# Kernel tuning notes

Hardware: AMD Instinct MI355X
Metric: run time of the kernel (lower is better)

The kernel has to match this reference:

```python
import jax, jax.numpy as jnp
import numpy as np
import math

N = 65536
C_IN = 64
C_OUT = 64
NS = 16
BN_EPS = 1e-5


def _knn_idx(p_np, k):
    # exact kNN (including self), chunked to bound memory
    p_np = np.asarray(p_np, np.float32)
    n = p_np.shape[0]
    sq = (p_np * p_np).sum(1)
    idx = np.empty((n, k), np.int32)
    cs = 1024
    for s in range(0, n, cs):
        q = p_np[s:s + cs]
        d = sq[None, :] - 2.0 * (q @ p_np.T) + (q * q).sum(1)[:, None]
        part = np.argpartition(d, k, axis=1)[:, :k]
        dd = np.take_along_axis(d, part, 1)
        order = np.argsort(dd, axis=1)
        idx[s:s + cs] = np.take_along_axis(part, order, 1).astype(np.int32)
    return idx


def setup_inputs() -> dict:
    key = jax.random.key(0)
    ks = jax.random.split(key, 12)
    p = jax.random.uniform(ks[0], (N, 3), dtype=jnp.float32) * 10.0
    x = jax.random.normal(ks[1], (N, C_IN), dtype=jnp.float32)
    idx = jnp.asarray(_knn_idx(np.asarray(p), NS))  # (N, NS) int32
    s_in = 1.0 / math.sqrt(C_IN)
    Wq = jax.random.normal(ks[2], (C_IN, C_OUT), dtype=jnp.float32) * s_in
    bq = jnp.zeros((C_OUT,), jnp.float32)
    Wk = jax.random.normal(ks[3], (C_IN, C_OUT), dtype=jnp.float32) * s_in
    bk = jnp.zeros((C_OUT,), jnp.float32)
    Wv = jax.random.normal(ks[4], (C_IN, C_OUT), dtype=jnp.float32) * s_in
    bv = jnp.zeros((C_OUT,), jnp.float32)
    Wp1 = jax.random.normal(ks[5], (3, 3), dtype=jnp.float32) * (1.0 / math.sqrt(3))
    bp1 = jnp.zeros((3,), jnp.float32)
    gamma = jnp.ones((3,), jnp.float32)
    beta = jnp.zeros((3,), jnp.float32)
    Wp2 = jax.random.normal(ks[6], (3, C_OUT), dtype=jnp.float32) * (1.0 / math.sqrt(3))
    bp2 = jnp.zeros((C_OUT,), jnp.float32)
    return {"p": p, "x": x, "idx": idx, "Wq": Wq, "bq": bq, "Wk": Wk, "bk": bk,
            "Wv": Wv, "bv": bv, "Wp1": Wp1, "bp1": bp1, "gamma": gamma,
            "beta": beta, "Wp2": Wp2, "bp2": bp2}


def reference(p, x, idx, Wq, bq, Wk, bk, Wv, bv, Wp1, bp1, gamma, beta, Wp2, bp2):
    x_q = x @ Wq + bq                       # (N, Co)
    x_k = (x @ Wk + bk)[idx]                # gather: (N, NS, Co)
    x_v = (x @ Wv + bv)[idx]                # gather: (N, NS, Co)
    p_r = p[idx] - p[:, None, :]            # relative coords (N, NS, 3)
    # linear_p: Linear(3,3) -> BatchNorm1d(3) (training stats) -> ReLU -> Linear(3,Co)
    h = p_r @ Wp1 + bp1                     # (N, NS, 3)
    mean = h.mean(axis=(0, 1))
    var = ((h - mean) ** 2).mean(axis=(0, 1))
    h = (h - mean) * jax.lax.rsqrt(var + BN_EPS) * gamma + beta
    h = jax.nn.relu(h)
    p_emb = h @ Wp2 + bp2                   # (N, NS, Co)
    x_k = x_k + p_emb
    x_v = x_v + p_emb
    attn = (x_q[:, None, :] * x_k).sum(-1) / math.sqrt(C_OUT)  # (N, NS)
    w = jax.nn.softmax(attn, axis=1)
    return (x_v * w[:, :, None]).sum(axis=1)  # (N, Co)
```

## Files before the change

kernel.cpp:

```cpp
#include <hip/hip_runtime.h>

#define N_PTS 65536
#define NSS 16

typedef __attribute__((ext_vector_type(8))) short short8;
typedef __attribute__((ext_vector_type(4))) float f32x4;

__device__ __forceinline__ unsigned short f2bf(float v) {
  unsigned int u = __float_as_uint(v);
  u += 0x7fffu + ((u >> 16) & 1u);
  return (unsigned short)(u >> 16);
}
__device__ __forceinline__ unsigned int pk2(float lo, float hi) {
  return (unsigned int)f2bf(lo) | ((unsigned int)f2bf(hi) << 16);
}
__device__ __forceinline__ float bflo(unsigned int u) { return __uint_as_float(u << 16); }
__device__ __forceinline__ float bfhi(unsigned int u) { return __uint_as_float(u & 0xffff0000u); }

union BF8 { int4 i; short8 s; };
union BU  { ushort4 u[2]; short8 s; };

__global__ __launch_bounds__(256, 3) void qkv_kernel(
    const float* __restrict__ x,
    const float* __restrict__ Wq, const float* __restrict__ Wk, const float* __restrict__ Wv,
    const float* __restrict__ bq, const float* __restrict__ bk, const float* __restrict__ bv,
    const float* __restrict__ Wp2, const float* __restrict__ bp2,
    const float* __restrict__ p, const int* __restrict__ idx,
    unsigned short* __restrict__ kvq, float* __restrict__ tq, float* __restrict__ statsP) {
  __shared__ __align__(16) unsigned short wtl[192 * 68];
  __shared__ __align__(16) unsigned short kvs[64 * 192];
  __shared__ __align__(16) unsigned short b2s[5 * 64];
  const int t = threadIdx.x, blk = blockIdx.x;
  const int p0 = blk * 64;
  const int lane = t & 63, wave = t >> 6;
  const int quad = lane >> 4, lr = lane & 15;

  const int pn = p0 + (t >> 2);
  const int4 j4 = ((const int4*)idx)[pn * 4 + (t & 3)];
  const float pnx = p[pn * 3 + 0], pny = p[pn * 3 + 1], pnz = p[pn * 3 + 2];
  const int js[4] = {j4.x, j4.y, j4.z, j4.w};
  float jx[4], jy[4], jz[4];
#pragma unroll
  for (int i = 0; i < 4; ++i) {
    jx[i] = p[js[i] * 3 + 0]; jy[i] = p[js[i] * 3 + 1]; jz[i] = p[js[i] * 3 + 2];
  }

#pragma unroll 8
  for (int i = 0; i < 48; ++i) {
    const int id = i * 256 + t;
    const int mat = id >> 12, rem = id & 4095;
    const int k = rem >> 6, n = rem & 63;
    const float* W = mat == 0 ? Wq : (mat == 1 ? Wk : Wv);
    wtl[(mat * 64 + n) * 68 + k] = f2bf(W[k * 64 + n]);
  }
  {
    const int row = t >> 6, c = t & 63;
    b2s[t] = f2bf(row < 3 ? Wp2[row * 64 + c] : bp2[c]);
    if (t < 64) b2s[256 + t] = 0;
  }
  __syncthreads();

  const int mrow = p0 + wave * 16 + lr;
  const float* xrow = x + (size_t)mrow * 64;
  const float4 fa = *(const float4*)(xrow + quad * 8);
  const float4 fb = *(const float4*)(xrow + quad * 8 + 4);
  const float4 fc = *(const float4*)(xrow + 32 + quad * 8);
  const float4 fd = *(const float4*)(xrow + 32 + quad * 8 + 4);
  BF8 ua, ub;
  ua.i = make_int4(pk2(fa.x, fa.y), pk2(fa.z, fa.w), pk2(fb.x, fb.y), pk2(fb.z, fb.w));
  ub.i = make_int4(pk2(fc.x, fc.y), pk2(fc.z, fc.w), pk2(fd.x, fd.y), pk2(fd.z, fd.w));
  const short8 a0 = ua.s;
  const short8 a1 = ub.s;

#pragma unroll
  for (int nt = 0; nt < 12; ++nt) {
    const unsigned short* bpr = wtl + (nt * 16 + lr) * 68 + quad * 8;
    BU B0, B1;
    B0.u[0] = *(const ushort4*)bpr;        B0.u[1] = *(const ushort4*)(bpr + 4);
    B1.u[0] = *(const ushort4*)(bpr + 32); B1.u[1] = *(const ushort4*)(bpr + 36);
    f32x4 acc = {0.f, 0.f, 0.f, 0.f};
    acc = __builtin_amdgcn_mfma_f32_16x16x32_bf16(a0, B0.s, acc, 0, 0, 0);
    acc = __builtin_amdgcn_mfma_f32_16x16x32_bf16(a1, B1.s, acc, 0, 0, 0);
    const int mat = nt >> 2;
    const int c = (nt & 3) * 16 + lr;
    const float bias = (mat == 0 ? bq : (mat == 1 ? bk : bv))[c];
#pragma unroll
    for (int r = 0; r < 4; ++r) {
      const int row = wave * 16 + quad * 4 + r;
      kvs[row * 192 + mat * 64 + c] = f2bf(acc[r] + bias);
    }
  }
  {
    const unsigned short* qp = kvs + (wave * 16 + lr) * 192;
    const short8 a0q = *(const short8*)(qp + quad * 8);
    const short8 a1q = *(const short8*)(qp + quad * 8 + 32);
    const unsigned short* b2p = b2s + (lr < 4 ? lr : 4) * 64 + quad * 8;
    const short8 b0q = *(const short8*)b2p;
    const short8 b1q = *(const short8*)(b2p + 32);
    f32x4 acc = {0.f, 0.f, 0.f, 0.f};
    acc = __builtin_amdgcn_mfma_f32_16x16x32_bf16(a0q, b0q, acc, 0, 0, 0);
    acc = __builtin_amdgcn_mfma_f32_16x16x32_bf16(a1q, b1q, acc, 0, 0, 0);
    if (lr < 4) {
#pragma unroll
      for (int r = 0; r < 4; ++r) {
        const int pt = p0 + wave * 16 + quad * 4 + r;
        tq[pt * 4 + lr] = acc[r];
      }
    }
  }

  float s0 = 0, s1 = 0, s2 = 0, s00 = 0, s01 = 0, s02 = 0, s11 = 0, s12 = 0, s22 = 0;
#pragma unroll
  for (int i = 0; i < 4; ++i) {
    const float dx = jx[i] - pnx, dy = jy[i] - pny, dz = jz[i] - pnz;
    s0 += dx; s1 += dy; s2 += dz;
    s00 += dx * dx; s01 += dx * dy; s02 += dx * dz;
    s11 += dy * dy; s12 += dy * dz; s22 += dz * dz;
  }
#pragma unroll
  for (int m = 1; m < 64; m <<= 1) {
    s0 += __shfl_xor(s0, m, 64);  s1 += __shfl_xor(s1, m, 64);  s2 += __shfl_xor(s2, m, 64);
    s00 += __shfl_xor(s00, m, 64); s01 += __shfl_xor(s01, m, 64); s02 += __shfl_xor(s02, m, 64);
    s11 += __shfl_xor(s11, m, 64); s12 += __shfl_xor(s12, m, 64); s22 += __shfl_xor(s22, m, 64);
  }

  __syncthreads();

  const uint4* kvs4 = (const uint4*)kvs;
  uint4* dst = (uint4*)(kvq + (size_t)p0 * 192);
#pragma unroll
  for (int j = 0; j < 6; ++j) dst[j * 256 + t] = kvs4[j * 256 + t];

  float* part = (float*)b2s;
  if (lane == 0) {
    part[wave * 9 + 0] = s0;  part[wave * 9 + 1] = s1;  part[wave * 9 + 2] = s2;
    part[wave * 9 + 3] = s00; part[wave * 9 + 4] = s01; part[wave * 9 + 5] = s02;
    part[wave * 9 + 6] = s11; part[wave * 9 + 7] = s12; part[wave * 9 + 8] = s22;
  }
  __syncthreads();
  if (t < 9) {
    statsP[t * 1024 + blk] = part[t] + part[9 + t] + part[18 + t] + part[27 + t];
  }
}

template <int CTRL>
__device__ __forceinline__ float dppmv(float x) {
  return __int_as_float(__builtin_amdgcn_update_dpp(
      __float_as_int(x), __float_as_int(x), CTRL, 0xF, 0xF, true));
}
__device__ __forceinline__ float red16_add(float x) {
  x += dppmv<0xB1>(x);
  x += dppmv<0x4E>(x);
  x += __shfl_xor(x, 4, 64);
  x += __shfl_xor(x, 8, 64);
  return x;
}
__device__ __forceinline__ float red16_max(float x) {
  x = fmaxf(x, dppmv<0xB1>(x));
  x = fmaxf(x, dppmv<0x4E>(x));
  x = fmaxf(x, __shfl_xor(x, 4, 64));
  x = fmaxf(x, __shfl_xor(x, 8, 64));
  return x;
}

__global__ __launch_bounds__(256, 4) void attn_kernel(
    const float* __restrict__ p, const int* __restrict__ idx,
    const unsigned short* __restrict__ kvq, const float* __restrict__ tq,
    const float* __restrict__ statsP,
    const float* __restrict__ Wp1, const float* __restrict__ bp1,
    const float* __restrict__ gamma, const float* __restrict__ beta,
    const float* __restrict__ Wp2, const float* __restrict__ bp2,
    float* __restrict__ out) {
  __shared__ float red[4][9];
  __shared__ float ebn_s[12];
  const int t = threadIdx.x, blk = blockIdx.x;
  const int lane = t & 63, wave = t >> 6;
  const int quad = lane >> 4, lr = lane & 15;

  {
    float s[9];
#pragma unroll
    for (int c = 0; c < 9; ++c) s[c] = 0.f;
#pragma unroll
    for (int i = 0; i < 4; ++i) {
      const int bI = i * 256 + t;
#pragma unroll
      for (int c = 0; c < 9; ++c) s[c] += statsP[c * 1024 + bI];
    }
#pragma unroll
    for (int m = 1; m < 64; m <<= 1) {
#pragma unroll
      for (int c = 0; c < 9; ++c) s[c] += __shfl_xor(s[c], m, 64);
    }
    if (lane == 0) {
#pragma unroll
      for (int c = 0; c < 9; ++c) red[wave][c] = s[c];
    }
    __syncthreads();
    if (t == 0) {
      float tot[9];
#pragma unroll
      for (int c = 0; c < 9; ++c) tot[c] = red[0][c] + red[1][c] + red[2][c] + red[3][c];
      const float invM = 1.0f / 1048576.0f;
      const float m0 = tot[0] * invM, m1 = tot[1] * invM, m2 = tot[2] * invM;
      const float cv00 = tot[3] * invM - m0 * m0, cv01 = tot[4] * invM - m0 * m1;
      const float cv02 = tot[5] * invM - m0 * m2, cv11 = tot[6] * invM - m1 * m1;
      const float cv12 = tot[7] * invM - m1 * m2, cv22 = tot[8] * invM - m2 * m2;
#pragma unroll
      for (int tt = 0; tt < 3; ++tt) {
        const float w0 = Wp1[0 * 3 + tt], w1 = Wp1[1 * 3 + tt], w2 = Wp1[2 * 3 + tt];
        const float mh = w0 * m0 + w1 * m1 + w2 * m2 + bp1[tt];
        const float var = w0 * w0 * cv00 + w1 * w1 * cv11 + w2 * w2 * cv22 +
                          2.f * (w0 * w1 * cv01 + w0 * w2 * cv02 + w1 * w2 * cv12);
        const float sc = gamma[tt] * rsqrtf(var + 1e-5f);
        ebn_s[tt] = w0 * sc; ebn_s[3 + tt] = w1 * sc; ebn_s[6 + tt] = w2 * sc;
        ebn_s[9 + tt] = (bp1[tt] - mh) * sc + beta[tt];
      }
    }
    __syncthreads();
  }

  float e[12];
#pragma unroll
  for (int i = 0; i < 12; ++i) e[i] = ebn_s[i];
  const float4 w20 = ((const float4*)Wp2)[lr];
  const float4 w21 = ((const float4*)Wp2)[16 + lr];
  const float4 w22 = ((const float4*)Wp2)[32 + lr];
  const float4 b2v = ((const float4*)bp2)[lr];

#pragma unroll 1
  for (int it = 0; it < 4; ++it) {
    const int base = blk * 64 + wave * 16 + it * 4;
    const int nown = base + quad;

    const int jg0 = idx[(base + 0) * NSS + lr];
    const int jg1 = idx[(base + 1) * NSS + lr];
    const int jg2 = idx[(base + 2) * NSS + lr];
    const int jg3 = idx[(base + 3) * NSS + lr];
    const int jall = quad == 0 ? jg0 : (quad == 1 ? jg1 : (quad == 2 ? jg2 : jg3));

    uint2 v[16];
    {
      const int4* idxr = (const int4*)(idx + (size_t)nown * NSS);
      const int4 ja = idxr[0], jb = idxr[1], jc = idxr[2], jd = idxr[3];
      const int jns[16] = {ja.x, ja.y, ja.z, ja.w, jb.x, jb.y, jb.z, jb.w,
                           jc.x, jc.y, jc.z, jc.w, jd.x, jd.y, jd.z, jd.w};
#pragma unroll
      for (int s = 0; s < NSS; ++s)
        v[s] = *(const uint2*)(kvq + (size_t)jns[s] * 192 + 128 + lr * 4);
    }

    const float pnx = p[nown * 3 + 0], pny = p[nown * 3 + 1], pnz = p[nown * 3 + 2];
    const float dx = p[jall * 3 + 0] - pnx;
    const float dy = p[jall * 3 + 1] - pny;
    const float dz = p[jall * 3 + 2] - pnz;
    const float4 t4 = ((const float4*)tq)[nown];

    float S = 0.f;
#pragma unroll
    for (int g = 0; g < 4; ++g) {
      const int jg = g == 0 ? jg0 : (g == 1 ? jg1 : (g == 2 ? jg2 : jg3));
      const short8 a0 = *(const short8*)(kvq + (size_t)(base + g) * 192 + quad * 8);
      const short8 a1 = *(const short8*)(kvq + (size_t)(base + g) * 192 + quad * 8 + 32);
      const short8 k0 = *(const short8*)(kvq + (size_t)jg * 192 + 64 + quad * 8);
      const short8 k1 = *(const short8*)(kvq + (size_t)jg * 192 + 64 + quad * 8 + 32);
      f32x4 acc = {0.f, 0.f, 0.f, 0.f};
      acc = __builtin_amdgcn_mfma_f32_16x16x32_bf16(a0, k0, acc, 0, 0, 0);
      acc = __builtin_amdgcn_mfma_f32_16x16x32_bf16(a1, k1, acc, 0, 0, 0);
      S = (quad == g) ? acc[0] : S;
    }

    const float h0 = fmaxf(fmaf(dx, e[0], fmaf(dy, e[3], fmaf(dz, e[6], e[9]))), 0.f);
    const float h1 = fmaxf(fmaf(dx, e[1], fmaf(dy, e[4], fmaf(dz, e[7], e[10]))), 0.f);
    const float h2 = fmaxf(fmaf(dx, e[2], fmaf(dy, e[5], fmaf(dz, e[8], e[11]))), 0.f);

    const float a = (S + fmaf(h0, t4.x, fmaf(h1, t4.y, fmaf(h2, t4.z, t4.w)))) * 0.125f;
    const float mx = red16_max(a);
    const float ex = __expf(a - mx);
    const float den = red16_add(ex);
    const float w = ex / den;

    const float H0 = red16_add(w * h0);
    const float H1 = red16_add(w * h1);
    const float H2 = red16_add(w * h2);

    float o0 = 0.f, o1 = 0.f, o2 = 0.f, o3 = 0.f;
#pragma unroll
    for (int s = 0; s < NSS; ++s) {
      const float ws = __shfl(w, (lane & 48) | s, 64);
      o0 = fmaf(ws, bflo(v[s].x), o0);
      o1 = fmaf(ws, bfhi(v[s].x), o1);
      o2 = fmaf(ws, bflo(v[s].y), o2);
      o3 = fmaf(ws, bfhi(v[s].y), o3);
    }

    o0 += fmaf(H0, w20.x, fmaf(H1, w21.x, fmaf(H2, w22.x, b2v.x)));
    o1 += fmaf(H0, w20.y, fmaf(H1, w21.y, fmaf(H2, w22.y, b2v.y)));
    o2 += fmaf(H0, w20.z, fmaf(H1, w21.z, fmaf(H2, w22.z, b2v.z)));
    o3 += fmaf(H0, w20.w, fmaf(H1, w21.w, fmaf(H2, w22.w, b2v.w)));
    const float4 res = {o0, o1, o2, o3};
    ((float4*)out)[nown * 16 + lr] = res;
  }
}

extern "C" void kernel_launch(void* const* d_in, const int* in_sizes, int n_in,
                              void* d_out, int out_size, void* d_ws, size_t ws_size,
                              hipStream_t stream) {
  const float* p     = (const float*)d_in[0];
  const float* x     = (const float*)d_in[1];
  const int*   idx   = (const int*)d_in[2];
  const float* Wq    = (const float*)d_in[3];
  const float* bq    = (const float*)d_in[4];
  const float* Wk    = (const float*)d_in[5];
  const float* bk    = (const float*)d_in[6];
  const float* Wv    = (const float*)d_in[7];
  const float* bv    = (const float*)d_in[8];
  const float* Wp1   = (const float*)d_in[9];
  const float* bp1   = (const float*)d_in[10];
  const float* gamma = (const float*)d_in[11];
  const float* beta  = (const float*)d_in[12];
  const float* Wp2   = (const float*)d_in[13];
  const float* bp2   = (const float*)d_in[14];
  float* out = (float*)d_out;

  char* w = (char*)d_ws;
  float* statsP       = (float*)w;
  unsigned short* kvq = (unsigned short*)(w + 65536);
  float* tq           = (float*)(w + 25231360);

  qkv_kernel<<<1024, 256, 0, stream>>>(x, Wq, Wk, Wv, bq, bk, bv, Wp2, bp2, p, idx,
                                       kvq, tq, statsP);
  attn_kernel<<<1024, 256, 0, stream>>>(p, idx, kvq, tq, statsP, Wp1, bp1, gamma, beta,
                                        Wp2, bp2, out);
}
```

Measured before the change: 155.4 us.

## Process points in Morton-ordered spatial cells to improve gather locality

Computes a 4096-cell Morton cell id for each point in the qkv kernel. A single-block prep kernel then builds a histogram and prefix offsets and folds in the BN statistics, and a scatter kernel builds a permutation. The attention kernel walks points in that spatially sorted order, with a block swizzle across XCDs, so neighbour K/V gathers hit cache more often. It adds two extra launches, including a serial one-block histogram with 65536 shared atomics, plus indirection through perm.

```diff
diff --git a/kernel.cpp b/kernel.cpp
--- a/kernel.cpp
+++ b/kernel.cpp
@@ -19,6 +19,18 @@
 
 union BF8 { int4 i; short8 s; };
 union BU  { ushort4 u[2]; short8 s; };
+
+__device__ __forceinline__ int cell_of(float px, float py, float pz) {
+  const int cx = min(15, max(0, (int)(px * 1.6f)));
+  const int cy = min(15, max(0, (int)(py * 1.6f)));
+  const int cz = min(15, max(0, (int)(pz * 1.6f)));
+  int m = 0;
+#pragma unroll
+  for (int b = 0; b < 4; ++b)
+    m |= (((cx >> b) & 1) << (3 * b + 2)) | (((cy >> b) & 1) << (3 * b + 1)) |
+         (((cz >> b) & 1) << (3 * b));
+  return m;
+}
 
 __global__ __launch_bounds__(256, 3) void qkv_kernel(
     const float* __restrict__ x,
@@ -26,7 +38,8 @@
     const float* __restrict__ bq, const float* __restrict__ bk, const float* __restrict__ bv,
     const float* __restrict__ Wp2, const float* __restrict__ bp2,
     const float* __restrict__ p, const int* __restrict__ idx,
-    unsigned short* __restrict__ kvq, float* __restrict__ tq, float* __restrict__ statsP) {
+    unsigned short* __restrict__ kvq, float* __restrict__ tq, float* __restrict__ statsP,
+    int* __restrict__ cellid) {
   __shared__ __align__(16) unsigned short wtl[192 * 68];
   __shared__ __align__(16) unsigned short kvs[64 * 192];
   __shared__ __align__(16) unsigned short b2s[5 * 64];
@@ -44,6 +57,7 @@
   for (int i = 0; i < 4; ++i) {
     jx[i] = p[js[i] * 3 + 0]; jy[i] = p[js[i] * 3 + 1]; jz[i] = p[js[i] * 3 + 2];
   }
+  if ((t & 3) == 0) cellid[pn] = cell_of(pnx, pny, pnz);
 
 #pragma unroll 8
   for (int i = 0; i < 48; ++i) {
@@ -143,6 +157,95 @@
   }
 }
 
+__global__ __launch_bounds__(256) void prep_kernel(
+    const int* __restrict__ cellid, const float* __restrict__ statsP,
+    const float* __restrict__ Wp1, const float* __restrict__ bp1,
+    const float* __restrict__ gamma, const float* __restrict__ beta,
+    float* __restrict__ ebn, int* __restrict__ offs) {
+  __shared__ int h[4096];
+  __shared__ int wtot[4];
+  __shared__ float red[4][9];
+  const int t = threadIdx.x;
+  const int lane = t & 63, wv = t >> 6;
+
+#pragma unroll
+  for (int i = 0; i < 16; ++i) h[i * 256 + t] = 0;
+  __syncthreads();
+#pragma unroll 4
+  for (int i = 0; i < 256; ++i) atomicAdd(&h[cellid[i * 256 + t]], 1);
+  __syncthreads();
+
+  int loc[16];
+  int sum = 0;
+#pragma unroll
+  for (int i = 0; i < 16; ++i) { loc[i] = h[t * 16 + i]; sum += loc[i]; }
+  int incl = sum;
+#pragma unroll
+  for (int off = 1; off < 64; off <<= 1) {
+    const int v = __shfl_up(incl, off, 64);
+    if (lane >= off) incl += v;
+  }
+  if (lane == 63) wtot[wv] = incl;
+  __syncthreads();
+  int wbase = 0;
+#pragma unroll
+  for (int i = 0; i < 4; ++i) wbase += (i < wv) ? wtot[i] : 0;
+  int run = wbase + incl - sum;
+#pragma unroll
+  for (int i = 0; i < 16; ++i) { offs[t * 16 + i] = run; run += loc[i]; }
+
+  float s[9];
+#pragma unroll
+  for (int c = 0; c < 9; ++c) s[c] = 0.f;
+#pragma unroll
+  for (int i = 0; i < 4; ++i) {
+#pragma unroll
+    for (int c = 0; c < 9; ++c) s[c] += statsP[c * 1024 + i * 256 + t];
+  }
+#pragma unroll
+  for (int m = 1; m < 64; m <<= 1) {
+#pragma unroll
+    for (int c = 0; c < 9; ++c) s[c] += __shfl_xor(s[c], m, 64);
+  }
+  if (lane == 0) {
+#pragma unroll
+    for (int c = 0; c < 9; ++c) red[wv][c] = s[c];
+  }
+  __syncthreads();
+  if (t == 0) {
+    float tot[9];
+#pragma unroll
+    for (int c = 0; c < 9; ++c) tot[c] = red[0][c] + red[1][c] + red[2][c] + red[3][c];
+    const float invM = 1.0f / 1048576.0f;
+    const float m0 = tot[0] * invM, m1 = tot[1] * invM, m2 = tot[2] * invM;
+    const float cv00 = tot[3] * invM - m0 * m0, cv01 = tot[4] * invM - m0 * m1;
+    const float cv02 = tot[5] * invM - m0 * m2, cv11 = tot[6] * invM - m1 * m1;
+    const float cv12 = tot[7] * invM - m1 * m2, cv22 = tot[8] * invM - m2 * m2;
+#pragma unroll
+    for (int tt = 0; tt < 3; ++tt) {
+      const float w0 = Wp1[0 * 3 + tt], w1 = Wp1[1 * 3 + tt], w2 = Wp1[2 * 3 + tt];
+      const float mh = w0 * m0 + w1 * m1 + w2 * m2 + bp1[tt];
+      const float var = w0 * w0 * cv00 + w1 * w1 * cv11 + w2 * w2 * cv22 +
+                        2.f * (w0 * w1 * cv01 + w0 * w2 * cv02 + w1 * w2 * cv12);
+      const float sc = gamma[tt] * rsqrtf(var + 1e-5f);
+      ebn[tt] = w0 * sc; ebn[3 + tt] = w1 * sc; ebn[6 + tt] = w2 * sc;
+      ebn[9 + tt] = (bp1[tt] - mh) * sc + beta[tt];
+    }
+  }
+}
+
+__global__ __launch_bounds__(256) void scatter_kernel(const int* __restrict__ cellid,
+                                                      int* __restrict__ offs,
+                                                      int* __restrict__ perm) {
+  const int tid = blockIdx.x * 256 + threadIdx.x;
+#pragma unroll
+  for (int j = 0; j < 4; ++j) {
+    const int n = tid + j * 16384;
+    const int pos = atomicAdd(&offs[cellid[n]], 1);
+    perm[pos] = n;
+  }
+}
+
 template <int CTRL>
 __device__ __forceinline__ float dppmv(float x) {
   return __int_as_float(__builtin_amdgcn_update_dpp(
@@ -166,63 +269,17 @@
 __global__ __launch_bounds__(256, 4) void attn_kernel(
     const float* __restrict__ p, const int* __restrict__ idx,
     const unsigned short* __restrict__ kvq, const float* __restrict__ tq,
-    const float* __restrict__ statsP,
-    const float* __restrict__ Wp1, const float* __restrict__ bp1,
-    const float* __restrict__ gamma, const float* __restrict__ beta,
+    const int* __restrict__ perm, const float* __restrict__ ebn,
     const float* __restrict__ Wp2, const float* __restrict__ bp2,
     float* __restrict__ out) {
-  __shared__ float red[4][9];
-  __shared__ float ebn_s[12];
   const int t = threadIdx.x, blk = blockIdx.x;
   const int lane = t & 63, wave = t >> 6;
   const int quad = lane >> 4, lr = lane & 15;
-
-  {
-    float s[9];
-#pragma unroll
-    for (int c = 0; c < 9; ++c) s[c] = 0.f;
-#pragma unroll
-    for (int i = 0; i < 4; ++i) {
-      const int bI = i * 256 + t;
-#pragma unroll
-      for (int c = 0; c < 9; ++c) s[c] += statsP[c * 1024 + bI];
-    }
-#pragma unroll
-    for (int m = 1; m < 64; m <<= 1) {
-#pragma unroll
-      for (int c = 0; c < 9; ++c) s[c] += __shfl_xor(s[c], m, 64);
-    }
-    if (lane == 0) {
-#pragma unroll
-      for (int c = 0; c < 9; ++c) red[wave][c] = s[c];
-    }
-    __syncthreads();
-    if (t == 0) {
-      float tot[9];
-#pragma unroll
-      for (int c = 0; c < 9; ++c) tot[c] = red[0][c] + red[1][c] + red[2][c] + red[3][c];
-      const float invM = 1.0f / 1048576.0f;
-      const float m0 = tot[0] * invM, m1 = tot[1] * invM, m2 = tot[2] * invM;
-      const float cv00 = tot[3] * invM - m0 * m0, cv01 = tot[4] * invM - m0 * m1;
-      const float cv02 = tot[5] * invM - m0 * m2, cv11 = tot[6] * invM - m1 * m1;
-      const float cv12 = tot[7] * invM - m1 * m2, cv22 = tot[8] * invM - m2 * m2;
-#pragma unroll
-      for (int tt = 0; tt < 3; ++tt) {
-        const float w0 = Wp1[0 * 3 + tt], w1 = Wp1[1 * 3 + tt], w2 = Wp1[2 * 3 + tt];
-        const float mh = w0 * m0 + w1 * m1 + w2 * m2 + bp1[tt];
-        const float var = w0 * w0 * cv00 + w1 * w1 * cv11 + w2 * w2 * cv22 +
-                          2.f * (w0 * w1 * cv01 + w0 * w2 * cv02 + w1 * w2 * cv12);
-        const float sc = gamma[tt] * rsqrtf(var + 1e-5f);
-        ebn_s[tt] = w0 * sc; ebn_s[3 + tt] = w1 * sc; ebn_s[6 + tt] = w2 * sc;
-        ebn_s[9 + tt] = (bp1[tt] - mh) * sc + beta[tt];
-      }
-    }
-    __syncthreads();
-  }
+  const int sb = (blk & 7) * 128 + (blk >> 3);
 
   float e[12];
 #pragma unroll
-  for (int i = 0; i < 12; ++i) e[i] = ebn_s[i];
+  for (int i = 0; i < 12; ++i) e[i] = ebn[i];
   const float4 w20 = ((const float4*)Wp2)[lr];
   const float4 w21 = ((const float4*)Wp2)[16 + lr];
   const float4 w22 = ((const float4*)Wp2)[32 + lr];
@@ -230,13 +287,15 @@
 
 #pragma unroll 1
   for (int it = 0; it < 4; ++it) {
-    const int base = blk * 64 + wave * 16 + it * 4;
-    const int nown = base + quad;
-
-    const int jg0 = idx[(base + 0) * NSS + lr];
-    const int jg1 = idx[(base + 1) * NSS + lr];
-    const int jg2 = idx[(base + 2) * NSS + lr];
-    const int jg3 = idx[(base + 3) * NSS + lr];
+    const int base = sb * 64 + wave * 16 + it * 4;
+    const int4 ng4 = *(const int4*)(perm + base);
+    const int ng[4] = {ng4.x, ng4.y, ng4.z, ng4.w};
+    const int nown = ng[quad];
+
+    const int jg0 = idx[ng4.x * NSS + lr];
+    const int jg1 = idx[ng4.y * NSS + lr];
+    const int jg2 = idx[ng4.z * NSS + lr];
+    const int jg3 = idx[ng4.w * NSS + lr];
     const int jall = quad == 0 ? jg0 : (quad == 1 ? jg1 : (quad == 2 ? jg2 : jg3));
 
     uint2 v[16];
@@ -260,8 +319,8 @@
 #pragma unroll
     for (int g = 0; g < 4; ++g) {
       const int jg = g == 0 ? jg0 : (g == 1 ? jg1 : (g == 2 ? jg2 : jg3));
-      const short8 a0 = *(const short8*)(kvq + (size_t)(base + g) * 192 + quad * 8);
-      const short8 a1 = *(const short8*)(kvq + (size_t)(base + g) * 192 + quad * 8 + 32);
+      const short8 a0 = *(const short8*)(kvq + (size_t)ng[g] * 192 + quad * 8);
+      const short8 a1 = *(const short8*)(kvq + (size_t)ng[g] * 192 + quad * 8 + 32);
       const short8 k0 = *(const short8*)(kvq + (size_t)jg * 192 + 64 + quad * 8);
       const short8 k1 = *(const short8*)(kvq + (size_t)jg * 192 + 64 + quad * 8 + 32);
       f32x4 acc = {0.f, 0.f, 0.f, 0.f};
@@ -325,11 +384,16 @@
 
   char* w = (char*)d_ws;
   float* statsP       = (float*)w;
-  unsigned short* kvq = (unsigned short*)(w + 65536);
-  float* tq           = (float*)(w + 25231360);
+  int* cellid         = (int*)(w + 40960);
+  int* offs           = (int*)(w + 303104);
+  float* ebn          = (float*)(w + 319488);
+  int* perm           = (int*)(w + 327680);
+  unsigned short* kvq = (unsigned short*)(w + 655360);
+  float* tq           = (float*)(w + 25821184);
 
   qkv_kernel<<<1024, 256, 0, stream>>>(x, Wq, Wk, Wv, bq, bk, bv, Wp2, bp2, p, idx,
-                                       kvq, tq, statsP);
-  attn_kernel<<<1024, 256, 0, stream>>>(p, idx, kvq, tq, statsP, Wp1, bp1, gamma, beta,
-                                        Wp2, bp2, out);
-}
+                                       kvq, tq, statsP, cellid);
+  prep_kernel<<<1, 256, 0, stream>>>(cellid, statsP, Wp1, bp1, gamma, beta, ebn, offs);
+  scatter_kernel<<<64, 256, 0, stream>>>(cellid, offs, perm);
+  attn_kernel<<<1024, 256, 0, stream>>>(p, idx, kvq, tq, perm, ebn, Wp2, bp2, out);
+}
```

Result: slower. 222.7 us (+43.3%).
